# Kernel tuning notes

Hardware: AMD Instinct MI355X
Metric: run time of the kernel (lower is better)

The kernel has to match this reference:

```python
import jax, jax.numpy as jnp
import numpy as np

N_QUBITS = 10
QLCU_LAYERS = 2
FEATURE_DIM = 256
BATCH = 256
N_PARAMS = 5 * N_QUBITS * QLCU_LAYERS  # 100
TWO_PI = 2.0 * np.pi


def _rx_mat(theta):
    # (B,) -> (B,2,2) complex64
    c = jnp.cos(theta / 2).astype(jnp.complex64)
    s = (-1j * jnp.sin(theta / 2)).astype(jnp.complex64)
    return jnp.stack([jnp.stack([c, s], -1), jnp.stack([s, c], -1)], -2)


def _ry_mat(theta):
    c = jnp.cos(theta / 2).astype(jnp.complex64)
    s = jnp.sin(theta / 2).astype(jnp.complex64)
    return jnp.stack([jnp.stack([c, -s], -1), jnp.stack([s, c], -1)], -2)


def _rz_mat(theta):
    e0 = jnp.exp(-0.5j * theta.astype(jnp.complex64))
    e1 = jnp.exp(0.5j * theta.astype(jnp.complex64))
    z = jnp.zeros_like(e0)
    return jnp.stack([jnp.stack([e0, z], -1), jnp.stack([z, e1], -1)], -2)


def _apply_1q(state, U, w):
    # state: (B,)+(2,)*n ; U: (B,2,2) ; wire w (PennyLane wire 0 = most significant)
    s = jnp.moveaxis(state, 1 + w, -1)
    s = jnp.einsum('bij,b...j->b...i', U, s)
    return jnp.moveaxis(s, -1, 1 + w)


def _apply_crx(state, theta, c, t):
    # controlled-RX: apply RX(theta) on target t where control c == 1
    s = jnp.moveaxis(state, (1 + c, 1 + t), (-2, -1))
    U = _rx_mat(theta)
    s1 = jnp.einsum('bij,b...j->b...i', U, s[..., 1, :])
    s = jnp.stack([s[..., 0, :], s1], axis=-2)
    return jnp.moveaxis(s, (-2, -1), (1 + c, 1 + t))


def _circuit(params):
    # params: (B, N_PARAMS) angles. Returns (B, 3*n) expvals [X.., Y.., Z..]
    n = N_QUBITS
    B = params.shape[0]
    state = jnp.zeros((B,) + (2,) * n, jnp.complex64)
    state = state.at[(slice(None),) + (0,) * n].set(1.0)
    idx = 0
    for _ in range(QLCU_LAYERS):
        for i in range(n):
            state = _apply_1q(state, _rx_mat(params[:, idx]), i)
            state = _apply_1q(state, _ry_mat(params[:, idx + 1]), i)
            state = _apply_1q(state, _rz_mat(params[:, idx + 2]), i)
            idx += 3
        for i in range(n):
            state = _apply_crx(state, params[:, idx], i, (i + 1) % n)
            idx += 1
        for i in range(n - 1, -1, -1):
            state = _apply_crx(state, params[:, idx], i, (i - 1) % n)
            idx += 1
    X, Y, Z = [], [], []
    for w in range(n):
        s = jnp.moveaxis(state, 1 + w, -1).reshape(B, -1, 2)
        z01 = jnp.sum(jnp.conj(s[..., 0]) * s[..., 1], axis=1)  # (B,)
        X.append(2.0 * jnp.real(z01))
        Y.append(2.0 * jnp.imag(z01))
        probs = jnp.sum(jnp.abs(s) ** 2, axis=1)  # (B,2)
        Z.append(probs[:, 0] - probs[:, 1])
    return jnp.stack(X + Y + Z, axis=1).astype(jnp.float32)


def _branch(x, W, b, base):
    p = x @ W.T + b            # (B, N_PARAMS)
    p = p + base[None, :]
    p = jax.nn.sigmoid(p) * TWO_PI
    return _circuit(p)


def setup_inputs() -> dict:
    key = jax.random.key(0)
    ks = jax.random.split(key, 16)
    d = {
        'x': jax.random.normal(ks[0], (BATCH, FEATURE_DIM), jnp.float32),
        'W1': jax.random.normal(ks[1], (N_PARAMS, FEATURE_DIM), jnp.float32) * 0.05,
        'b1': jnp.zeros((N_PARAMS,), jnp.float32),
        'W2': jax.random.normal(ks[2], (N_PARAMS, FEATURE_DIM), jnp.float32) * 0.05,
        'b2': jnp.zeros((N_PARAMS,), jnp.float32),
        'W3': jax.random.normal(ks[3], (N_PARAMS, FEATURE_DIM), jnp.float32) * 0.05,
        'b3': jnp.zeros((N_PARAMS,), jnp.float32),
        'base1': jax.random.uniform(ks[4], (N_PARAMS,), jnp.float32) * TWO_PI,
        'base2': jax.random.uniform(ks[5], (N_PARAMS,), jnp.float32) * TWO_PI,
        'base3': jax.random.uniform(ks[6], (N_PARAMS,), jnp.float32) * TWO_PI,
        'alpha_real': jax.random.uniform(ks[7], (1,), jnp.float32),
        'alpha_imag': jnp.zeros((1,), jnp.float32),
        'beta_real': jax.random.uniform(ks[8], (1,), jnp.float32),
        'beta_imag': jnp.zeros((1,), jnp.float32),
        'gamma_real': jax.random.uniform(ks[9], (1,), jnp.float32),
        'gamma_imag': jnp.zeros((1,), jnp.float32),
    }
    return d


def reference(x, W1, b1, W2, b2, W3, b3, base1, base2, base3,
              alpha_real, alpha_imag, beta_real, beta_imag, gamma_real, gamma_imag):
    m1 = _branch(x, W1, b1, base1)  # (B, 3n)
    m2 = _branch(x, W2, b2, base2)
    m3 = _branch(x, W3, b3, base3)
    norm = jnp.sqrt(alpha_real**2 + alpha_imag**2 + beta_real**2 + beta_imag**2
                    + gamma_real**2 + gamma_imag**2 + 1e-9)
    ar, ai = alpha_real / norm, alpha_imag / norm
    br, bi = beta_real / norm, beta_imag / norm
    gr, gi = gamma_real / norm, gamma_imag / norm
    re = ar * m1 + br * m2 + gr * m3
    im = ai * m1 + bi * m2 + gi * m3
    return jnp.sqrt(re * re + im * im)
```

## Files before the change

### kernel.cpp

```cpp
#include <hip/hip_runtime.h>
#include <math.h>

#define NQ 10
#define NSTATE 1024
#define NPAR 100
#define FDIM 256
#define BATCH 256
#define NOUT 30
#define TWO_PI_F 6.283185307179586f

__device__ __forceinline__ float2 cmul(float2 a, float2 b) {
    return make_float2(fmaf(a.x, b.x, -a.y*b.y), fmaf(a.x, b.y, a.y*b.x));
}
__device__ __forceinline__ float2 cadd(float2 a, float2 b) {
    return make_float2(a.x + b.x, a.y + b.y);
}

__device__ __forceinline__ void crx_gate(float2* st, float2 cshalf, int bc, int bt, int tid) {
    const float c = cshalf.x, s = cshalf.y;
    const int b_lo = bc < bt ? bc : bt;
    const int b_hi = bc < bt ? bt : bc;
    int i = tid;
    i = ((i >> b_lo) << (b_lo + 1)) | (i & ((1 << b_lo) - 1));
    i = ((i >> b_hi) << (b_hi + 1)) | (i & ((1 << b_hi) - 1));
    const int i0 = i | (1 << bc);
    const int i1 = i0 | (1 << bt);
    float2 a0 = st[i0], a1 = st[i1];
    st[i0] = make_float2(fmaf(c, a0.x,  s * a1.y), fmaf(c, a0.y, -s * a1.x));
    st[i1] = make_float2(fmaf(c, a1.x,  s * a0.y), fmaf(c, a1.y, -s * a0.x));
    __syncthreads();
}

__global__ __launch_bounds__(256) void qsb_branch(
    const float* __restrict__ x,
    const float* __restrict__ W1, const float* __restrict__ b1, const float* __restrict__ base1,
    const float* __restrict__ W2, const float* __restrict__ b2, const float* __restrict__ base2,
    const float* __restrict__ W3, const float* __restrict__ b3, const float* __restrict__ base3,
    float* __restrict__ m_ws)
{
    const int b   = blockIdx.x;
    const int br  = blockIdx.y;
    const int tid = threadIdx.x;

    const float* W    = (br == 0) ? W1    : (br == 1) ? W2    : W3;
    const float* bias = (br == 0) ? b1    : (br == 1) ? b2    : b3;
    const float* base = (br == 0) ? base1 : (br == 1) ? base2 : base3;
    float* m_out = m_ws + (size_t)br * (BATCH * NOUT);

    __shared__ float  xrow[FDIM];
    __shared__ float2 cs[NPAR];
    __shared__ float2 st[NSTATE];
    __shared__ float  redA[4], redB[4], redC[4];

    xrow[tid] = x[(size_t)b * FDIM + tid];
    __syncthreads();

    if (tid < NPAR) {
        const float* wr = W + (size_t)tid * FDIM;
        float acc = 0.f;
        #pragma unroll 8
        for (int k = 0; k < FDIM; ++k) acc = fmaf(xrow[k], wr[k], acc);
        acc += bias[tid] + base[tid];
        float p = TWO_PI_F / (1.f + expf(-acc));
        float sh, ch;
        __sincosf(0.5f * p, &sh, &ch);
        cs[tid] = make_float2(ch, sh);
    }
    for (int i = tid; i < NSTATE; i += 256)
        st[i] = make_float2(i == 0 ? 1.f : 0.f, 0.f);
    __syncthreads();

    int idx = 0;
    for (int layer = 0; layer < 2; ++layer) {
        for (int q = 0; q < NQ; ++q) {
            const float2 X = cs[idx], Y = cs[idx + 1], Z = cs[idx + 2];
            idx += 3;
            const float cx = X.x, sx = X.y, cy = Y.x, sy = Y.y, cz = Z.x, sz = Z.y;
            const float2 m00 = make_float2( cy * cx,  sy * sx);
            const float2 m01 = make_float2(-sy * cx, -cy * sx);
            const float2 m10 = make_float2( sy * cx, -cy * sx);
            const float2 m11 = make_float2( cy * cx, -sy * sx);
            const float2 z0 = make_float2(cz, -sz), z1 = make_float2(cz, sz);
            const float2 u00 = cmul(z0, m00), u01 = cmul(z0, m01);
            const float2 u10 = cmul(z1, m10), u11 = cmul(z1, m11);

            const int bpos = 9 - q;
            const int bit  = 1 << bpos;
            #pragma unroll
            for (int pp = 0; pp < 2; ++pp) {
                const int p   = tid + pp * 256;
                const int low = p & (bit - 1);
                const int i0  = ((p ^ low) << 1) | low;
                const int i1  = i0 | bit;
                float2 a0 = st[i0], a1 = st[i1];
                float2 n0 = cadd(cmul(u00, a0), cmul(u01, a1));
                float2 n1 = cadd(cmul(u10, a0), cmul(u11, a1));
                st[i0] = n0; st[i1] = n1;
            }
            __syncthreads();
        }
        for (int q = 0; q < NQ; ++q) {
            crx_gate(st, cs[idx], 9 - q, 9 - ((q + 1) % NQ), tid);
            idx++;
        }
        for (int q = NQ - 1; q >= 0; --q) {
            crx_gate(st, cs[idx], 9 - q, 9 - ((q + NQ - 1) % NQ), tid);
            idx++;
        }
    }

    const int wv = tid >> 6, lane = tid & 63;
    for (int w = 0; w < NQ; ++w) {
        const int bpos = 9 - w;
        const int bit  = 1 << bpos;
        float sre = 0.f, sim = 0.f, szz = 0.f;
        #pragma unroll
        for (int pp = 0; pp < 2; ++pp) {
            const int p   = tid + pp * 256;
            const int low = p & (bit - 1);
            const int i0  = ((p ^ low) << 1) | low;
            const int i1  = i0 | bit;
            float2 a0 = st[i0], a1 = st[i1];
            sre += a0.x * a1.x + a0.y * a1.y;
            sim += a0.x * a1.y - a0.y * a1.x;
            szz += (a0.x * a0.x + a0.y * a0.y) - (a1.x * a1.x + a1.y * a1.y);
        }
        #pragma unroll
        for (int off = 32; off > 0; off >>= 1) {
            sre += __shfl_down(sre, off, 64);
            sim += __shfl_down(sim, off, 64);
            szz += __shfl_down(szz, off, 64);
        }
        if (lane == 0) { redA[wv] = sre; redB[wv] = sim; redC[wv] = szz; }
        __syncthreads();
        if (tid == 0) {
            const float Xv = 2.f * (redA[0] + redA[1] + redA[2] + redA[3]);
            const float Yv = 2.f * (redB[0] + redB[1] + redB[2] + redB[3]);
            const float Zv = redC[0] + redC[1] + redC[2] + redC[3];
            m_out[(size_t)b * NOUT + w]      = Xv;
            m_out[(size_t)b * NOUT + 10 + w] = Yv;
            m_out[(size_t)b * NOUT + 20 + w] = Zv;
        }
        __syncthreads();
    }
}

__global__ __launch_bounds__(256) void qsb_combine(
    const float* __restrict__ m,
    const float* __restrict__ ar_, const float* __restrict__ ai_,
    const float* __restrict__ br_, const float* __restrict__ bi_,
    const float* __restrict__ gr_, const float* __restrict__ gi_,
    float* __restrict__ out)
{
    const int i = blockIdx.x * blockDim.x + threadIdx.x;
    if (i >= BATCH * NOUT) return;
    const float ar = ar_[0], ai = ai_[0];
    const float br = br_[0], bi = bi_[0];
    const float gr = gr_[0], gi = gi_[0];
    const float inv = 1.f / sqrtf(ar*ar + ai*ai + br*br + bi*bi + gr*gr + gi*gi + 1e-9f);
    const float m1 = m[i];
    const float m2 = m[BATCH * NOUT + i];
    const float m3 = m[2 * BATCH * NOUT + i];
    const float re = (ar * m1 + br * m2 + gr * m3) * inv;
    const float im = (ai * m1 + bi * m2 + gi * m3) * inv;
    out[i] = sqrtf(re * re + im * im);
}

extern "C" void kernel_launch(void* const* d_in, const int* in_sizes, int n_in,
                              void* d_out, int out_size, void* d_ws, size_t ws_size,
                              hipStream_t stream)
{
    (void)in_sizes; (void)n_in; (void)out_size; (void)ws_size;
    const float* x     = (const float*)d_in[0];
    const float* W1    = (const float*)d_in[1];
    const float* b1    = (const float*)d_in[2];
    const float* W2    = (const float*)d_in[3];
    const float* b2    = (const float*)d_in[4];
    const float* W3    = (const float*)d_in[5];
    const float* b3    = (const float*)d_in[6];
    const float* base1 = (const float*)d_in[7];
    const float* base2 = (const float*)d_in[8];
    const float* base3 = (const float*)d_in[9];
    const float* ar    = (const float*)d_in[10];
    const float* ai    = (const float*)d_in[11];
    const float* br    = (const float*)d_in[12];
    const float* bi    = (const float*)d_in[13];
    const float* gr    = (const float*)d_in[14];
    const float* gi    = (const float*)d_in[15];

    float* m_ws = (float*)d_ws;
    float* out  = (float*)d_out;

    dim3 grid(BATCH, 3), block(256);
    qsb_branch<<<grid, block, 0, stream>>>(x, W1, b1, base1, W2, b2, base2,
                                           W3, b3, base3, m_ws);
    qsb_combine<<<(BATCH * NOUT + 255) / 256, 256, 0, stream>>>(
        m_ws, ar, ai, br, bi, gr, gi, out);
}
```

Before: 121.7 us.

## Hold statevector in registers of one wavefront, use lane shuffles for gates

Each simulation now runs in a single 64-lane wavefront. The 1024-amplitude state is spread across 16 registers per lane, so low-bit gates use cross-lane xor shuffles and high-bit gates are register-local, all unrolled at compile time through templates. This removes the shared-memory state and the per-gate __syncthreads barriers, and the measurement reduction becomes a wave-level butterfly. The angle projection is also vectorised to float4 loads with two parameters per lane, reading x straight from global memory. In exchange, fewer threads work on each simulation, register pressure rises, and the weight-projection phase has lower parallelism.

```diff
diff --git a/kernel.cpp b/kernel.cpp
--- a/kernel.cpp
+++ b/kernel.cpp
@@ -2,147 +2,256 @@
 #include <math.h>
 
 #define NQ 10
-#define NSTATE 1024
 #define NPAR 100
 #define FDIM 256
 #define BATCH 256
 #define NOUT 30
 #define TWO_PI_F 6.283185307179586f
 
-__device__ __forceinline__ float2 cmul(float2 a, float2 b) {
-    return make_float2(fmaf(a.x, b.x, -a.y*b.y), fmaf(a.x, b.y, a.y*b.x));
-}
-__device__ __forceinline__ float2 cadd(float2 a, float2 b) {
-    return make_float2(a.x + b.x, a.y + b.y);
-}
-
-__device__ __forceinline__ void crx_gate(float2* st, float2 cshalf, int bc, int bt, int tid) {
-    const float c = cshalf.x, s = cshalf.y;
-    const int b_lo = bc < bt ? bc : bt;
-    const int b_hi = bc < bt ? bt : bc;
-    int i = tid;
-    i = ((i >> b_lo) << (b_lo + 1)) | (i & ((1 << b_lo) - 1));
-    i = ((i >> b_hi) << (b_hi + 1)) | (i & ((1 << b_hi) - 1));
-    const int i0 = i | (1 << bc);
-    const int i1 = i0 | (1 << bt);
-    float2 a0 = st[i0], a1 = st[i1];
-    st[i0] = make_float2(fmaf(c, a0.x,  s * a1.y), fmaf(c, a0.y, -s * a1.x));
-    st[i1] = make_float2(fmaf(c, a1.x,  s * a0.y), fmaf(c, a1.y, -s * a0.x));
-    __syncthreads();
-}
-
-__global__ __launch_bounds__(256) void qsb_branch(
+
+__device__ __forceinline__ float shx(float v, int mask) {
+    return __shfl_xor(v, mask, 64);
+}
+
+template<int BIT>
+__device__ __forceinline__ void gate1q(float2 (&st)[16], int lane,
+                                       float2 u00, float2 u01, float2 u10, float2 u11)
+{
+    if constexpr (BIT >= 6) {
+        constexpr int rb = 1 << (BIT - 6);
+        #pragma unroll
+        for (int a = 0; a < 16; ++a) {
+            if (a & rb) continue;
+            const int a1 = a | rb;
+            const float2 A0 = st[a], A1 = st[a1];
+            float2 n0, n1;
+            n0.x = u00.x*A0.x - u00.y*A0.y + u01.x*A1.x - u01.y*A1.y;
+            n0.y = u00.x*A0.y + u00.y*A0.x + u01.x*A1.y + u01.y*A1.x;
+            n1.x = u10.x*A0.x - u10.y*A0.y + u11.x*A1.x - u11.y*A1.y;
+            n1.y = u10.x*A0.y + u10.y*A0.x + u11.x*A1.y + u11.y*A1.x;
+            st[a] = n0; st[a1] = n1;
+        }
+    } else {
+        constexpr int lb = 1 << BIT;
+        const bool hi = (lane & lb) != 0;
+        const float2 A = hi ? u11 : u00;
+        const float2 B = hi ? u10 : u01;
+        #pragma unroll
+        for (int a = 0; a < 16; ++a) {
+            const float2 m = st[a];
+            float2 p;
+            p.x = shx(m.x, lb); p.y = shx(m.y, lb);
+            float2 n;
+            n.x = A.x*m.x - A.y*m.y + B.x*p.x - B.y*p.y;
+            n.y = A.x*m.y + A.y*m.x + B.x*p.y + B.y*p.x;
+            st[a] = n;
+        }
+    }
+}
+
+template<int BC, int BT>
+__device__ __forceinline__ void crx(float2 (&st)[16], int lane, float c, float s)
+{
+    if constexpr (BT >= 6) {
+        constexpr int rt = 1 << (BT - 6);
+        if constexpr (BC >= 6) {
+            constexpr int rc = 1 << (BC - 6);
+            #pragma unroll
+            for (int a = 0; a < 16; ++a) {
+                if (!(a & rc) || (a & rt)) continue;
+                const int a1 = a | rt;
+                const float2 A0 = st[a], A1 = st[a1];
+                float2 n0, n1;
+                n0.x = c*A0.x + s*A1.y;  n0.y = c*A0.y - s*A1.x;
+                n1.x = c*A1.x + s*A0.y;  n1.y = c*A1.y - s*A0.x;
+                st[a] = n0; st[a1] = n1;
+            }
+        } else {
+            constexpr int lc = 1 << BC;
+            const bool act = (lane & lc) != 0;
+            const float cc = act ? c : 1.f;
+            const float ss = act ? s : 0.f;
+            #pragma unroll
+            for (int a = 0; a < 16; ++a) {
+                if (a & rt) continue;
+                const int a1 = a | rt;
+                const float2 A0 = st[a], A1 = st[a1];
+                float2 n0, n1;
+                n0.x = cc*A0.x + ss*A1.y;  n0.y = cc*A0.y - ss*A1.x;
+                n1.x = cc*A1.x + ss*A0.y;  n1.y = cc*A1.y - ss*A0.x;
+                st[a] = n0; st[a1] = n1;
+            }
+        }
+    } else {
+        constexpr int lt = 1 << BT;
+        float cc, ss;
+        if constexpr (BC < 6) {
+            constexpr int lc = 1 << BC;
+            const bool act = (lane & lc) != 0;
+            cc = act ? c : 1.f;
+            ss = act ? s : 0.f;
+        } else { cc = c; ss = s; }
+        #pragma unroll
+        for (int a = 0; a < 16; ++a) {
+            if constexpr (BC >= 6) {
+                constexpr int rc = 1 << (BC - 6);
+                if (!(a & rc)) continue;
+            }
+            const float2 m = st[a];
+            float2 p;
+            p.x = shx(m.x, lt); p.y = shx(m.y, lt);
+            float2 n;
+            n.x = cc*m.x + ss*p.y;
+            n.y = cc*m.y - ss*p.x;
+            st[a] = n;
+        }
+    }
+}
+
+template<int Q>
+__device__ __forceinline__ void layer1q(float2 (&st)[16], int lane, const float2* cs, int idx)
+{
+    if constexpr (Q < NQ) {
+        const float2 X = cs[idx], Y = cs[idx + 1], Z = cs[idx + 2];
+        const float cx = X.x, sx = X.y, cy = Y.x, sy = Y.y, cz = Z.x, sz = Z.y;
+        const float2 m00 = make_float2( cy*cx,  sy*sx);
+        const float2 m01 = make_float2(-sy*cx, -cy*sx);
+        const float2 m10 = make_float2( sy*cx, -cy*sx);
+        const float2 m11 = make_float2( cy*cx, -sy*sx);
+        const float2 u00 = make_float2(cz*m00.x + sz*m00.y, cz*m00.y - sz*m00.x);
+        const float2 u01 = make_float2(cz*m01.x + sz*m01.y, cz*m01.y - sz*m01.x);
+        const float2 u10 = make_float2(cz*m10.x - sz*m10.y, cz*m10.y + sz*m10.x);
+        const float2 u11 = make_float2(cz*m11.x - sz*m11.y, cz*m11.y + sz*m11.x);
+        gate1q<9 - Q>(st, lane, u00, u01, u10, u11);
+        layer1q<Q + 1>(st, lane, cs, idx + 3);
+    }
+}
+
+template<int Q>
+__device__ __forceinline__ void ringF(float2 (&st)[16], int lane, const float2* cs, int idx)
+{
+    if constexpr (Q < NQ) {
+        const float2 p = cs[idx];
+        crx<9 - Q, 9 - ((Q + 1) % NQ)>(st, lane, p.x, p.y);
+        ringF<Q + 1>(st, lane, cs, idx + 1);
+    }
+}
+
+template<int Q>
+__device__ __forceinline__ void ringB(float2 (&st)[16], int lane, const float2* cs, int idx)
+{
+    if constexpr (Q >= 0) {
+        const float2 p = cs[idx];
+        crx<9 - Q, 9 - ((Q + NQ - 1) % NQ)>(st, lane, p.x, p.y);
+        ringB<Q - 1>(st, lane, cs, idx + 1);
+    }
+}
+
+template<int W>
+__device__ __forceinline__ void measureAll(const float2 (&st)[16], int lane, float* m_row)
+{
+    if constexpr (W < NQ) {
+        constexpr int B = 9 - W;
+        float sre = 0.f, smm = 0.f, szz = 0.f;
+        if constexpr (B >= 6) {
+            constexpr int rb = 1 << (B - 6);
+            #pragma unroll
+            for (int a = 0; a < 16; ++a) {
+                if (a & rb) continue;
+                const int a1 = a | rb;
+                const float2 A0 = st[a], A1 = st[a1];
+                sre += A0.x*A1.x + A0.y*A1.y;
+                smm += A0.x*A1.y - A0.y*A1.x;
+                szz += A0.x*A0.x + A0.y*A0.y - A1.x*A1.x - A1.y*A1.y;
+            }
+            sre *= 2.f; smm *= 2.f;
+        } else {
+            constexpr int lb = 1 << B;
+            const float sgn = (lane & lb) ? -1.f : 1.f;
+            #pragma unroll
+            for (int a = 0; a < 16; ++a) {
+                const float2 m = st[a];
+                float2 p;
+                p.x = shx(m.x, lb); p.y = shx(m.y, lb);
+                sre += m.x*p.x + m.y*p.y;
+                smm += sgn * (m.x*p.y - m.y*p.x);
+                szz += sgn * (m.x*m.x + m.y*m.y - p.x*p.x - p.y*p.y);
+            }
+            szz *= 0.5f;
+        }
+        #pragma unroll
+        for (int off = 1; off < 64; off <<= 1) {
+            sre += shx(sre, off);
+            smm += shx(smm, off);
+            szz += shx(szz, off);
+        }
+        if (lane == 0) {
+            m_row[W]      = sre;
+            m_row[10 + W] = smm;
+            m_row[20 + W] = szz;
+        }
+        measureAll<W + 1>(st, lane, m_row);
+    }
+}
+
+__global__ __launch_bounds__(64) void qsb_branch(
     const float* __restrict__ x,
     const float* __restrict__ W1, const float* __restrict__ b1, const float* __restrict__ base1,
     const float* __restrict__ W2, const float* __restrict__ b2, const float* __restrict__ base2,
     const float* __restrict__ W3, const float* __restrict__ b3, const float* __restrict__ base3,
     float* __restrict__ m_ws)
 {
-    const int b   = blockIdx.x;
-    const int br  = blockIdx.y;
-    const int tid = threadIdx.x;
+    const int sim  = blockIdx.x;
+    const int b    = sim & (BATCH - 1);
+    const int br   = sim >> 8;
+    const int lane = threadIdx.x;
 
     const float* W    = (br == 0) ? W1    : (br == 1) ? W2    : W3;
     const float* bias = (br == 0) ? b1    : (br == 1) ? b2    : b3;
     const float* base = (br == 0) ? base1 : (br == 1) ? base2 : base3;
-    float* m_out = m_ws + (size_t)br * (BATCH * NOUT);
-
-    __shared__ float  xrow[FDIM];
+
     __shared__ float2 cs[NPAR];
-    __shared__ float2 st[NSTATE];
-    __shared__ float  redA[4], redB[4], redC[4];
-
-    xrow[tid] = x[(size_t)b * FDIM + tid];
+
+    if (lane < 50) {
+        const int p0 = 2 * lane;
+        const float4* xr = reinterpret_cast<const float4*>(x + (size_t)b * FDIM);
+        const float4* w0 = reinterpret_cast<const float4*>(W + (size_t)p0 * FDIM);
+        const float4* w1 = reinterpret_cast<const float4*>(W + (size_t)(p0 + 1) * FDIM);
+        float acc0 = 0.f, acc1 = 0.f;
+        #pragma unroll 8
+        for (int k = 0; k < FDIM / 4; ++k) {
+            const float4 xv = xr[k];
+            const float4 a  = w0[k];
+            const float4 bb = w1[k];
+            acc0 += xv.x*a.x  + xv.y*a.y  + xv.z*a.z  + xv.w*a.w;
+            acc1 += xv.x*bb.x + xv.y*bb.y + xv.z*bb.z + xv.w*bb.w;
+        }
+        acc0 += bias[p0]     + base[p0];
+        acc1 += bias[p0 + 1] + base[p0 + 1];
+        const float t0 = TWO_PI_F / (1.f + __expf(-acc0));
+        const float t1 = TWO_PI_F / (1.f + __expf(-acc1));
+        float s0, c0, s1, c1;
+        __sincosf(0.5f * t0, &s0, &c0);
+        __sincosf(0.5f * t1, &s1, &c1);
+        cs[p0]     = make_float2(c0, s0);
+        cs[p0 + 1] = make_float2(c1, s1);
+    }
     __syncthreads();
 
-    if (tid < NPAR) {
-        const float* wr = W + (size_t)tid * FDIM;
-        float acc = 0.f;
-        #pragma unroll 8
-        for (int k = 0; k < FDIM; ++k) acc = fmaf(xrow[k], wr[k], acc);
-        acc += bias[tid] + base[tid];
-        float p = TWO_PI_F / (1.f + expf(-acc));
-        float sh, ch;
-        __sincosf(0.5f * p, &sh, &ch);
-        cs[tid] = make_float2(ch, sh);
-    }
-    for (int i = tid; i < NSTATE; i += 256)
-        st[i] = make_float2(i == 0 ? 1.f : 0.f, 0.f);
-    __syncthreads();
-
-    int idx = 0;
-    for (int layer = 0; layer < 2; ++layer) {
-        for (int q = 0; q < NQ; ++q) {
-            const float2 X = cs[idx], Y = cs[idx + 1], Z = cs[idx + 2];
-            idx += 3;
-            const float cx = X.x, sx = X.y, cy = Y.x, sy = Y.y, cz = Z.x, sz = Z.y;
-            const float2 m00 = make_float2( cy * cx,  sy * sx);
-            const float2 m01 = make_float2(-sy * cx, -cy * sx);
-            const float2 m10 = make_float2( sy * cx, -cy * sx);
-            const float2 m11 = make_float2( cy * cx, -sy * sx);
-            const float2 z0 = make_float2(cz, -sz), z1 = make_float2(cz, sz);
-            const float2 u00 = cmul(z0, m00), u01 = cmul(z0, m01);
-            const float2 u10 = cmul(z1, m10), u11 = cmul(z1, m11);
-
-            const int bpos = 9 - q;
-            const int bit  = 1 << bpos;
-            #pragma unroll
-            for (int pp = 0; pp < 2; ++pp) {
-                const int p   = tid + pp * 256;
-                const int low = p & (bit - 1);
-                const int i0  = ((p ^ low) << 1) | low;
-                const int i1  = i0 | bit;
-                float2 a0 = st[i0], a1 = st[i1];
-                float2 n0 = cadd(cmul(u00, a0), cmul(u01, a1));
-                float2 n1 = cadd(cmul(u10, a0), cmul(u11, a1));
-                st[i0] = n0; st[i1] = n1;
-            }
-            __syncthreads();
-        }
-        for (int q = 0; q < NQ; ++q) {
-            crx_gate(st, cs[idx], 9 - q, 9 - ((q + 1) % NQ), tid);
-            idx++;
-        }
-        for (int q = NQ - 1; q >= 0; --q) {
-            crx_gate(st, cs[idx], 9 - q, 9 - ((q + NQ - 1) % NQ), tid);
-            idx++;
-        }
-    }
-
-    const int wv = tid >> 6, lane = tid & 63;
-    for (int w = 0; w < NQ; ++w) {
-        const int bpos = 9 - w;
-        const int bit  = 1 << bpos;
-        float sre = 0.f, sim = 0.f, szz = 0.f;
-        #pragma unroll
-        for (int pp = 0; pp < 2; ++pp) {
-            const int p   = tid + pp * 256;
-            const int low = p & (bit - 1);
-            const int i0  = ((p ^ low) << 1) | low;
-            const int i1  = i0 | bit;
-            float2 a0 = st[i0], a1 = st[i1];
-            sre += a0.x * a1.x + a0.y * a1.y;
-            sim += a0.x * a1.y - a0.y * a1.x;
-            szz += (a0.x * a0.x + a0.y * a0.y) - (a1.x * a1.x + a1.y * a1.y);
-        }
-        #pragma unroll
-        for (int off = 32; off > 0; off >>= 1) {
-            sre += __shfl_down(sre, off, 64);
-            sim += __shfl_down(sim, off, 64);
-            szz += __shfl_down(szz, off, 64);
-        }
-        if (lane == 0) { redA[wv] = sre; redB[wv] = sim; redC[wv] = szz; }
-        __syncthreads();
-        if (tid == 0) {
-            const float Xv = 2.f * (redA[0] + redA[1] + redA[2] + redA[3]);
-            const float Yv = 2.f * (redB[0] + redB[1] + redB[2] + redB[3]);
-            const float Zv = redC[0] + redC[1] + redC[2] + redC[3];
-            m_out[(size_t)b * NOUT + w]      = Xv;
-            m_out[(size_t)b * NOUT + 10 + w] = Yv;
-            m_out[(size_t)b * NOUT + 20 + w] = Zv;
-        }
-        __syncthreads();
-    }
+    float2 st[16];
+    #pragma unroll
+    for (int a = 0; a < 16; ++a) st[a] = make_float2(0.f, 0.f);
+    if (lane == 0) st[0].x = 1.f;
+
+    layer1q<0>(st, lane, cs, 0);
+    ringF<0>(st, lane, cs, 30);
+    ringB<NQ - 1>(st, lane, cs, 40);
+    layer1q<0>(st, lane, cs, 50);
+    ringF<0>(st, lane, cs, 80);
+    ringB<NQ - 1>(st, lane, cs, 90);
+
+    float* m_row = m_ws + ((size_t)br * BATCH + b) * NOUT;
+    measureAll<0>(st, lane, m_row);
 }
 
 __global__ __launch_bounds__(256) void qsb_combine(
@@ -191,9 +300,8 @@
     float* m_ws = (float*)d_ws;
     float* out  = (float*)d_out;
 
-    dim3 grid(BATCH, 3), block(256);
-    qsb_branch<<<grid, block, 0, stream>>>(x, W1, b1, base1, W2, b2, base2,
-                                           W3, b3, base3, m_ws);
+    qsb_branch<<<dim3(BATCH * 3), dim3(64), 0, stream>>>(
+        x, W1, b1, base1, W2, b2, base2, W3, b3, base3, m_ws);
     qsb_combine<<<(BATCH * NOUT + 255) / 256, 256, 0, stream>>>(
         m_ws, ar, ai, br, bi, gr, gi, out);
 }
```

Measured after the change: 125.7 us. 3.3% more time.
